# Kernel tuning notes

Hardware: AMD Instinct MI355X
Metric: run time of the kernel (lower is better)

Reference implementation:

```python
import jax, jax.numpy as jnp
import numpy as np

TIME_GAP_BUCKET_COUNT = 64

def setup_inputs() -> dict:
    key = jax.random.key(0)
    ks = jax.random.split(key, 16)
    B, L, H, V, M, G = 32, 512, 256, 100000, 1024, 8
    time_emb = jax.random.normal(ks[8], (TIME_GAP_BUCKET_COUNT + 1, H), jnp.float32) * 0.02
    group_emb = jax.random.normal(ks[9], (G + 1, H), jnp.float32) * 0.02
    return {
        'history_tokens': jax.random.randint(ks[0], (B, L), 0, V, jnp.int32),
        'history_post_tokens': jax.random.randint(ks[1], (B, L), 0, V, jnp.int32),
        'history_author_tokens': jax.random.randint(ks[2], (B, L), 0, V, jnp.int32),
        'history_action_tokens': jax.random.randint(ks[3], (B, L), 0, V, jnp.int32),
        'history_time_gap': jax.random.randint(ks[4], (B, L), 0, TIME_GAP_BUCKET_COUNT + 1, jnp.int32),
        'history_group_ids': jax.random.randint(ks[5], (B, L), 0, G + 1, jnp.int32),
        'history_mask': jax.random.randint(ks[6], (B, L), 0, 2, jnp.int32).astype(bool),
        'token_emb': jax.random.normal(ks[7], (V, H), jnp.float32) * 0.02,
        'time_emb': time_emb.at[0].set(0.0),   # padding_idx=0
        'group_emb': group_emb.at[0].set(0.0),  # padding_idx=0
        'pos_emb': jax.random.normal(ks[10], (M, H), jnp.float32) * 0.02,
        'sep_token': jax.random.normal(ks[11], (H,), jnp.float32) * 0.02,
        'ln_g': jnp.ones((6 * H,), jnp.float32),
        'ln_b': jnp.zeros((6 * H,), jnp.float32),
        'W1': jax.random.normal(ks[12], (6 * H, 4 * H), jnp.float32) * 0.02,
        'b1': jnp.zeros((4 * H,), jnp.float32),
        'W2': jax.random.normal(ks[13], (4 * H, H), jnp.float32) * 0.02,
        'b2': jnp.zeros((H,), jnp.float32),
    }

def _next_valid_group(gid, mask):
    # For each position i, group id of the nearest valid position j > i (or -1).
    B, L = gid.shape
    def step(carry, xm):
        g, m = xm
        return jnp.where(m, g, carry), carry  # emit pre-update carry
    _, nxt = jax.lax.scan(step, jnp.full((B,), -1, gid.dtype),
                          (jnp.flip(gid, 1).T, jnp.flip(mask, 1).T))  # [L,B]
    return jnp.flip(nxt.T, 1)

def reference(history_tokens, history_post_tokens, history_author_tokens,
              history_action_tokens, history_time_gap, history_group_ids,
              history_mask, token_emb, time_emb, group_emb, pos_emb,
              sep_token, ln_g, ln_b, W1, b1, W2, b2):
    M, H = pos_emb.shape
    B, L = history_mask.shape
    # --- event feature assembly ---
    feats = jnp.concatenate([
        token_emb[history_tokens], token_emb[history_post_tokens],
        token_emb[history_author_tokens], token_emb[history_action_tokens],
        time_emb[jnp.clip(history_time_gap, 0, TIME_GAP_BUCKET_COUNT)],
        group_emb[history_group_ids]], axis=-1)  # [B,L,6H]
    mu = feats.mean(-1, keepdims=True)
    var = feats.var(-1, keepdims=True)
    xn = (feats - mu) * jax.lax.rsqrt(var + 1e-5) * ln_g + ln_b
    ev = jax.nn.silu(xn @ W1 + b1) @ W2 + b2  # [B,L,H]
    # --- vectorized merge_with_sep ---
    gid, mask = history_group_ids, history_mask
    nxt = _next_valid_group(gid, mask)
    sep_valid = mask & (nxt >= 0) & (nxt != gid)
    sep_b = jnp.broadcast_to(sep_token, ev.shape)
    tok_c = jnp.stack([ev, sep_b], axis=2).reshape(B, 2 * L, H)   # event, then sep slot
    msk_c = jnp.stack([mask, sep_valid], axis=2).reshape(B, 2 * L)
    rank = jnp.cumsum(msk_c, axis=1) - 1                          # rank among valid pieces
    count = jnp.sum(msk_c, axis=1)                                # pieces per batch
    tgt = M - count[:, None] + rank                               # right-aligned target
    tgt = jnp.where(msk_c & (tgt >= 0), tgt, M)                   # overflow/invalid -> dump slot
    bidx = jnp.arange(B)[:, None]
    merged = jnp.zeros((B, M + 1, H), ev.dtype).at[bidx, tgt].set(
        jnp.where(msk_c[..., None], tok_c, 0.0))[:, :M]
    merged_mask = jnp.zeros((B, M + 1), bool).at[bidx, tgt].set(msk_c)[:, :M]
    merged = (merged + pos_emb[None]) * merged_mask[..., None].astype(ev.dtype)
    return merged, merged_mask
```

## Files before the change

kernel.cpp:

```cpp
#include <hip/hip_runtime.h>
#include <string.h>

#define Hh   256
#define SIXH 1536
#define Bb_  32
#define Ll_  512
#define BL_  16384
#define Mm_  1024
#define N1_  1024
#define K1_  1536
#define K2_  1024
#define N2_  256

typedef __attribute__((ext_vector_type(8))) short bf16x8;
typedef __attribute__((ext_vector_type(4))) float f32x4;

__device__ inline float bf2f(unsigned short u){ unsigned x=(unsigned)u<<16; float f; memcpy(&f,&x,4); return f; }
__device__ inline unsigned short f2bf(float f){ unsigned x; memcpy(&x,&f,4); x = x + 0x7FFFu + ((x>>16)&1u); return (unsigned short)(x>>16); }

#define GL16(gp, lp) __builtin_amdgcn_global_load_lds( \
    (const __attribute__((address_space(1))) void*)(gp), \
    (__attribute__((address_space(3))) void*)(lp), 16, 0, 0)

__global__ __launch_bounds__(256) void prep_kernel(
  const unsigned int* __restrict__ m, int* __restrict__ flag,
  const float* __restrict__ W1, unsigned short* __restrict__ W1t,
  const float* __restrict__ W2, unsigned short* __restrict__ W2t)
{
  int bidg = blockIdx.x;
  int t = threadIdx.x;
  if (bidg == 0){
    bool gt1=false, isf=false;
    for (int i=t;i<4096;i+=256){ unsigned v=m[i]; if(v>1u) gt1=true; if(v==0x3F800000u) isf=true; }
    unsigned long long bg = __ballot(gt1), bf = __ballot(isf);
    __shared__ unsigned long long s1[4], s2[4];
    int w = t>>6;
    if ((t&63)==0){ s1[w]=bg; s2[w]=bf; }
    __syncthreads();
    if (t==0){
      bool g = (s1[0]|s1[1]|s1[2]|s1[3])!=0ull;
      bool f = (s2[0]|s2[1]|s2[2]|s2[3])!=0ull;
      *flag = g ? (f?2:1) : 0;
    }
    return;
  }
  const float* W; unsigned short* Wt; int K, N, id;
  if (bidg <= (K1_/32)*(N1_/32)){ W = W1; Wt = W1t; K = K1_; N = N1_; id = bidg-1; }
  else { W = W2; Wt = W2t; K = K2_; N = N2_; id = bidg-1-(K1_/32)*(N1_/32); }
  __shared__ float tl[32][33];
  int ntx = N >> 5;
  int bx = id % ntx;
  int by = id / ntx;
  int tx = t & 31, ty = t >> 5;
  #pragma unroll
  for (int i=0;i<32;i+=8)
    tl[ty+i][tx] = W[(size_t)(by*32+ty+i)*N + bx*32+tx];
  __syncthreads();
  #pragma unroll
  for (int i=0;i<32;i+=8)
    Wt[(size_t)(bx*32+ty+i)*K + by*32+tx] = f2bf(tl[tx][ty+i]);
}

__global__ __launch_bounds__(256) void gather_ln2_kernel(
  const int* __restrict__ tok, const int* __restrict__ post,
  const int* __restrict__ auth, const int* __restrict__ act,
  const int* __restrict__ tg,  const int* __restrict__ gidp,
  const float* __restrict__ token_emb, const float* __restrict__ time_emb,
  const float* __restrict__ group_emb,
  const float* __restrict__ ln_g, const float* __restrict__ ln_b,
  unsigned short* __restrict__ xn)
{
  int t = threadIdx.x;
  int rib = t >> 7;
  int row = blockIdx.x*2 + rib;
  int wai = (t >> 6) & 1;
  int l   = t & 63;

  int e0 = wai ? post[row] : tok[row];
  int e1 = wai ? act[row]  : auth[row];
  const float* b2p;
  if (wai == 0){
    int i4 = tg[row]; i4 = (i4 < 0) ? 0 : (i4 > 64 ? 64 : i4);
    b2p = time_emb + (size_t)i4*Hh;
  } else {
    b2p = group_emb + (size_t)gidp[row]*Hh;
  }
  const float* b0p = token_emb + (size_t)e0*Hh;
  const float* b1p = token_emb + (size_t)e1*Hh;

  float4 v0 = *(const float4*)(b0p + l*4);
  float4 v1 = *(const float4*)(b1p + l*4);
  float4 v2 = *(const float4*)(b2p + l*4);

  float s  = v0.x+v0.y+v0.z+v0.w + v1.x+v1.y+v1.z+v1.w + v2.x+v2.y+v2.z+v2.w;
  float s2 = v0.x*v0.x+v0.y*v0.y+v0.z*v0.z+v0.w*v0.w
           + v1.x*v1.x+v1.y*v1.y+v1.z*v1.z+v1.w*v1.w
           + v2.x*v2.x+v2.y*v2.y+v2.z*v2.z+v2.w*v2.w;
  #pragma unroll
  for (int off=32; off; off>>=1){ s += __shfl_xor(s,off); s2 += __shfl_xor(s2,off); }

  __shared__ float rs[2][2], rq[2][2];
  if (l==0){ rs[rib][wai] = s; rq[rib][wai] = s2; }
  __syncthreads();
  s  = rs[rib][0] + rs[rib][1];
  s2 = rq[rib][0] + rq[rib][1];
  float mu   = s * (1.0f/1536.0f);
  float var  = s2 * (1.0f/1536.0f) - mu*mu;
  float rstd = rsqrtf(var + 1e-5f);

  unsigned short* xr = xn + (size_t)row*SIXH;
  #pragma unroll
  for (int p=0;p<3;p++){
    int seg = p*2 + wai;
    int j = seg*Hh + l*4;
    float4 g4 = *(const float4*)(ln_g + j);
    float4 bb = *(const float4*)(ln_b + j);
    float4 v = (p==0) ? v0 : (p==1) ? v1 : v2;
    ushort4 o;
    o.x = f2bf((v.x-mu)*rstd*g4.x + bb.x);
    o.y = f2bf((v.y-mu)*rstd*g4.y + bb.y);
    o.z = f2bf((v.z-mu)*rstd*g4.z + bb.z);
    o.w = f2bf((v.w-mu)*rstd*g4.w + bb.w);
    *(ushort4*)(xr + j) = o;
  }
}

__global__ __launch_bounds__(512, 2) void gemm1_cs_kernel(
  const unsigned short* __restrict__ A, const unsigned short* __restrict__ Bt,
  const float* __restrict__ bias, unsigned short* __restrict__ C,
  int M, int N, int K)
{
  __shared__ unsigned short lds[65536];

  int nbx = N >> 8;
  int bid = blockIdx.x;
  if ((gridDim.x & 7) == 0){
    int chunk = gridDim.x >> 3;
    bid = (bid & 7)*chunk + (bid >> 3);
  }
  int bx = bid % nbx, by = bid / nbx;
  int brow = by*256, bcol = bx*256;

  int tid = threadIdx.x, lane = tid & 63, wid = tid >> 6;
  int wr = wid >> 1, wc = wid & 1;

  int sRow = tid >> 3;
  int sSw  = ((tid & 7) ^ (sRow & 7)) << 3;
  const unsigned short* pA0 = A  + (size_t)(brow +   0 + sRow)*K + sSw;
  const unsigned short* pA1 = A  + (size_t)(brow +  64 + sRow)*K + sSw;
  const unsigned short* pA2 = A  + (size_t)(brow + 128 + sRow)*K + sSw;
  const unsigned short* pA3 = A  + (size_t)(brow + 192 + sRow)*K + sSw;
  const unsigned short* pB0 = Bt + (size_t)(bcol +   0 + sRow)*K + sSw;
  const unsigned short* pB1 = Bt + (size_t)(bcol +  64 + sRow)*K + sSw;
  const unsigned short* pB2 = Bt + (size_t)(bcol + 128 + sRow)*K + sSw;
  const unsigned short* pB3 = Bt + (size_t)(bcol + 192 + sRow)*K + sSw;

  int fr = lane & 15, kb = lane >> 4;
  int g0 = (kb ^ (fr & 3)) | (fr & 4);
  int aB = (wr*64  + fr)*64 + g0*8;
  int bB = (wc*128 + fr)*64 + g0*8;

  f32x4 acc[4][8];
  #pragma unroll
  for (int q=0;q<4;q++)
    #pragma unroll
    for (int n=0;n<8;n++) acc[q][n] = (f32x4){0.f,0.f,0.f,0.f};

  bf16x8 a0[4], a1[4], bP[4], bQ[4];

#define ABASE(S) ((S)*16384)
#define BBASE(S) (32768 + (S)*16384)

#define RD_A(buf, S, kc) do{ \
    const unsigned short* L_ = lds + ABASE(S) + (aB ^ ((kc)?32:0)); \
    buf[0] = *(const bf16x8*)(L_); \
    buf[1] = *(const bf16x8*)(L_ + 1024); \
    buf[2] = *(const bf16x8*)(L_ + 2048); \
    buf[3] = *(const bf16x8*)(L_ + 3072); }while(0)

#define RD_B(buf, S, h, kc) do{ \
    const unsigned short* L_ = lds + BBASE(S) + (h)*4096 + (bB ^ ((kc)?32:0)); \
    buf[0] = *(const bf16x8*)(L_); \
    buf[1] = *(const bf16x8*)(L_ + 1024); \
    buf[2] = *(const bf16x8*)(L_ + 2048); \
    buf[3] = *(const bf16x8*)(L_ + 3072); }while(0)

#define STG(p, DB, OFF) GL16((p) + (OFF), lds + (DB) + wid*512)

#define MMX(AF, BF, NB) do{ \
    _Pragma("unroll") for (int q=0;q<4;q++) \
      _Pragma("unroll") for (int nn=0;nn<4;nn++) \
        acc[q][(NB)+nn] = __builtin_amdgcn_mfma_f32_16x16x32_bf16( \
            AF[q], BF[nn], acc[q][(NB)+nn], 0, 0, 0); }while(0)

#define LGKM0 asm volatile("s_waitcnt lgkmcnt(0)" ::: "memory")
#define BAR  __builtin_amdgcn_s_barrier()
#define VM0  asm volatile("s_waitcnt vmcnt(0)" ::: "memory")
#define VNOP do{}while(0)

#define TILE(S, OB1, SP, V4) do{ \
    if (SP){ \
      STG(pA0, ABASE((S)^1) + 0,     OB1); \
      STG(pA1, ABASE((S)^1) + 4096,  OB1); \
      STG(pA2, ABASE((S)^1) + 8192,  OB1); \
      STG(pA3, ABASE((S)^1) + 12288, OB1); \
      STG(pB0, BBASE((S)^1) + 0,     OB1); \
      STG(pB1, BBASE((S)^1) + 4096,  OB1); \
      STG(pB2, BBASE((S)^1) + 8192,  OB1); \
      STG(pB3, BBASE((S)^1) + 12288, OB1); } \
    RD_A(a0, S, 0); RD_B(bP, S, 0, 0); RD_B(bQ, S, 1, 0); \
    MMX(a0, bP, 0); \
    RD_A(a1, S, 1); RD_B(bP, S, 1, 1); \
    MMX(a0, bQ, 4); \
    RD_B(bQ, S, 0, 1); \
    MMX(a1, bP, 4); \
    MMX(a1, bQ, 0); \
    LGKM0; V4; BAR; \
    asm volatile("" ::: "memory"); \
  }while(0)

  int nk = K >> 6;
  STG(pA0, ABASE(0)+0, 0);     STG(pA1, ABASE(0)+4096, 0);
  STG(pA2, ABASE(0)+8192, 0);  STG(pA3, ABASE(0)+12288, 0);
  STG(pB0, BBASE(0)+0, 0);     STG(pB1, BBASE(0)+4096, 0);
  STG(pB2, BBASE(0)+8192, 0);  STG(pB3, BBASE(0)+12288, 0);
  VM0; BAR;
  asm volatile("" ::: "memory");

  for (int tt = 0; tt < (nk-2)/2; ++tt){
    TILE(0,  64, 1, VM0);
    TILE(1, 128, 1, VM0);
    pA0 += 128; pA1 += 128; pA2 += 128; pA3 += 128;
    pB0 += 128; pB1 += 128; pB2 += 128; pB3 += 128;
  }
  TILE(0, 64, 1, VM0);
  TILE(1, 0, 0, VNOP);

#undef TILE
#undef RD_A
#undef RD_B
#undef STG
#undef MMX

  int colb = bcol + wc*128 + fr;
  float bv[8];
  #pragma unroll
  for (int n=0;n<8;n++) bv[n] = bias[colb + n*16];
  int r0 = brow + wr*64 + (lane>>4)*4;
  #pragma unroll
  for (int q=0;q<4;q++){
    #pragma unroll
    for (int j=0;j<4;j++){
      int r = r0 + q*16 + j;
      #pragma unroll
      for (int n=0;n<8;n++){
        float x = acc[q][n][j] + bv[n];
        x = x / (1.0f + expf(-x));
        C[(size_t)r*N + colb + n*16] = f2bf(x);
      }
    }
  }
}

__global__ __launch_bounds__(256) void gemm2_64_kernel(
  const unsigned short* __restrict__ A, const unsigned short* __restrict__ Bt,
  const float* __restrict__ bias, float* __restrict__ C,
  int M, int N, int K)
{
  __shared__ unsigned short As[4096];
  __shared__ unsigned short Bs[4096];
  int nbx = N >> 6;
  int bid = blockIdx.x;
  if ((gridDim.x & 7) == 0){
    int chunk = gridDim.x >> 3;
    bid = (bid & 7)*chunk + (bid >> 3);
  }
  int bx = bid % nbx, by = bid / nbx;
  int brow = by*64, bcol = bx*64;
  int tid = threadIdx.x, lane = tid & 63, wid = tid >> 6;
  int wr = wid >> 1, wc = wid & 1;

  int srow = tid >> 3;
  int sg   = ((tid & 7) ^ (srow & 7)) << 3;
  const unsigned short* pA0 = A  + (size_t)(brow + srow)*K + sg;
  const unsigned short* pA1 = pA0 + (size_t)32*K;
  const unsigned short* pB0 = Bt + (size_t)(bcol + srow)*K + sg;
  const unsigned short* pB1 = pB0 + (size_t)32*K;

  int fr = lane & 15, kb = lane >> 4;
  int g0 = (kb ^ (fr & 7)) << 3;
  int aB = (wr*32 + fr)*64 + g0;
  int bB = (wc*32 + fr)*64 + g0;

  f32x4 acc[2][2];
  #pragma unroll
  for (int i=0;i<2;i++)
    #pragma unroll
    for (int j=0;j<2;j++) acc[i][j] = (f32x4){0.f,0.f,0.f,0.f};

  for (int kt = 0; kt < K; kt += 64){
    GL16(pA0 + kt, As + wid*512);
    GL16(pA1 + kt, As + 2048 + wid*512);
    GL16(pB0 + kt, Bs + wid*512);
    GL16(pB1 + kt, Bs + 2048 + wid*512);
    __syncthreads();
    bf16x8 a[2][2], b[2][2];
    #pragma unroll
    for (int m=0;m<2;m++)
      #pragma unroll
      for (int kc=0;kc<2;kc++){
        a[m][kc] = *(const bf16x8*)(As + ((aB + m*1024) ^ (kc<<5)));
        b[m][kc] = *(const bf16x8*)(Bs + ((bB + m*1024) ^ (kc<<5)));
      }
    #pragma unroll
    for (int kc=0;kc<2;kc++)
      #pragma unroll
      for (int m=0;m<2;m++)
        #pragma unroll
        for (int n=0;n<2;n++)
          acc[m][n] = __builtin_amdgcn_mfma_f32_16x16x32_bf16(a[m][kc], b[n][kc], acc[m][n], 0, 0, 0);
    __syncthreads();
  }

  int col0 = bcol + wc*32 + fr;
  int row0 = brow + wr*32 + (lane >> 4)*4;
  #pragma unroll
  for (int m=0;m<2;m++){
    #pragma unroll
    for (int j=0;j<4;j++){
      int r = row0 + m*16 + j;
      #pragma unroll
      for (int n=0;n<2;n++){
        int c = col0 + n*16;
        C[(size_t)r*N + c] = acc[m][n][j] + bias[c];
      }
    }
  }
}

__global__ __launch_bounds__(512) void merge_meta_kernel(
  const void* __restrict__ maskp, const int* __restrict__ gid,
  const int* __restrict__ flag,
  int* __restrict__ src, int* __restrict__ count)
{
  int b = blockIdx.x;
  int i = threadIdx.x;
  int lane = i & 63, w = i >> 6;
  __shared__ int sg[Ll_];
  __shared__ int fv[8];
  __shared__ int wt[8];
  int f = *flag;
  int mv;
  if (f==0)      mv = ((const int*)maskp)[b*Ll_+i];
  else if (f==1) mv = ((const unsigned char*)maskp)[b*Ll_+i];
  else           mv = (((const float*)maskp)[b*Ll_+i] != 0.0f);
  bool m = (mv != 0);
  int g = gid[b*Ll_+i];
  sg[i] = g;
  unsigned long long W = __ballot(m);
  if (lane==0) fv[w] = W ? (w*64 + __builtin_ctzll(W)) : -1;
  __syncthreads();
  unsigned long long rem = (lane==63) ? 0ull : (W >> (lane+1));
  int nxtpos = -1;
  if (rem) nxtpos = w*64 + lane + 1 + __builtin_ctzll(rem);
  else {
    #pragma unroll
    for (int k=0;k<8;k++)
      if (nxtpos < 0 && k > w && fv[k] >= 0) nxtpos = fv[k];
  }
  int nxt = (nxtpos >= 0) ? sg[nxtpos] : -1;
  bool sep = m && (nxt >= 0) && (nxt != g);
  int ci = (m?1:0) + (sep?1:0);
  int v = ci;
  #pragma unroll
  for (int off=1; off<64; off<<=1){
    int u = __shfl_up(v, off);
    if (lane >= off) v += u;
  }
  if (lane==63) wt[w] = v;
  __syncthreads();
  int woff = 0;
  #pragma unroll
  for (int k=0;k<8;k++) if (k < w) woff += wt[k];
  int e = woff + v - ci;
  int* sb = src + b*Mm_;
  if (m){
    sb[e] = 2*i;
    if (sep) sb[e+1] = 2*i+1;
  }
  if (i==0){
    int tot=0;
    #pragma unroll
    for (int k=0;k<8;k++) tot += wt[k];
    count[b] = tot;
  }
}

__global__ __launch_bounds__(256) void output_kernel(
  const float* __restrict__ ev, const float* __restrict__ pos_emb,
  const float* __restrict__ sep_token,
  const int* __restrict__ src, const int* __restrict__ count,
  float* __restrict__ out)
{
  int tid  = threadIdx.x;
  int tpos = blockIdx.x*4 + (tid>>6);
  int lane = tid & 63;
  int b = tpos >> 10;
  int t = tpos & 1023;
  int cnt = count[b];
  int start = Mm_ - cnt;
  float4 val = make_float4(0.f,0.f,0.f,0.f);
  float maskv = 0.f;
  if (t >= start){
    maskv = 1.f;
    int slot = src[b*Mm_ + (t - start)];
    const float* sv = (slot & 1) ? sep_token
                                 : ev + (size_t)(b*Ll_ + (slot>>1))*Hh;
    float4 x = *(const float4*)(sv + lane*4);
    float4 p = *(const float4*)(pos_emb + (size_t)t*Hh + lane*4);
    val = make_float4(x.x+p.x, x.y+p.y, x.z+p.z, x.w+p.w);
  }
  *(float4*)(out + (size_t)tpos*Hh + lane*4) = val;
  if (lane==0) out[(size_t)Bb_*Mm_*Hh + tpos] = maskv;
}

extern "C" void kernel_launch(void* const* d_in, const int* in_sizes, int n_in,
                              void* d_out, int out_size, void* d_ws, size_t ws_size,
                              hipStream_t stream) {
  const int* tok    = (const int*)d_in[0];
  const int* post   = (const int*)d_in[1];
  const int* auth   = (const int*)d_in[2];
  const int* act    = (const int*)d_in[3];
  const int* tg     = (const int*)d_in[4];
  const int* gid    = (const int*)d_in[5];
  const void* maskp =             d_in[6];
  const float* token_emb = (const float*)d_in[7];
  const float* time_emb  = (const float*)d_in[8];
  const float* group_emb = (const float*)d_in[9];
  const float* pos_emb   = (const float*)d_in[10];
  const float* sep_token = (const float*)d_in[11];
  const float* ln_g = (const float*)d_in[12];
  const float* ln_b = (const float*)d_in[13];
  const float* W1   = (const float*)d_in[14];
  const float* b1   = (const float*)d_in[15];
  const float* W2   = (const float*)d_in[16];
  const float* b2   = (const float*)d_in[17];

  char* ws = (char*)d_ws;
  size_t off = 0;
  int* flag = (int*)ws;                                  off += 256;
  unsigned short* xn  = (unsigned short*)(ws + off);     off += (size_t)BL_*SIXH*2;
  unsigned short* h1  = (unsigned short*)(ws + off);     off += (size_t)BL_*N1_*2;
  float*          ev  = (float*)(ws + off);              off += (size_t)BL_*N2_*4;
  unsigned short* w1t = (unsigned short*)(ws + off);     off += (size_t)K1_*N1_*2;
  unsigned short* w2t = (unsigned short*)(ws + off);     off += (size_t)K2_*N2_*2;
  int*            src = (int*)(ws + off);                off += (size_t)Bb_*Mm_*4;
  int*            cnt = (int*)(ws + off);                off += 256;

  const int PREP_BLOCKS = 1 + (K1_/32)*(N1_/32) + (K2_/32)*(N2_/32);
  prep_kernel<<<PREP_BLOCKS,256,0,stream>>>((const unsigned int*)maskp, flag,
                                            W1, w1t, W2, w2t);
  gather_ln2_kernel<<<BL_/2,256,0,stream>>>(tok,post,auth,act,tg,gid,
                                            token_emb,time_emb,group_emb,
                                            ln_g,ln_b,xn);
  gemm1_cs_kernel<<<(BL_/256)*(N1_/256),512,0,stream>>>(
      xn, w1t, b1, h1, BL_, N1_, K1_);
  gemm2_64_kernel<<<(BL_/64)*(N2_/64),256,0,stream>>>(
      h1, w2t, b2, ev, BL_, N2_, K2_);
  merge_meta_kernel<<<Bb_,512,0,stream>>>(maskp, gid, flag, src, cnt);
  output_kernel<<<(Bb_*Mm_)/4,256,0,stream>>>(ev, pos_emb, sep_token, src, cnt, (float*)d_out);
}
```

Measured before the change: 114.4 us.

## Fuse prep, gather-LN and merge-meta into one kernel; double-buffer GEMM2

Merges the weight transpose/convert, mask-format detection, the embedding gather with LayerNorm, and the merge metadata scan into a single 512-thread launch, partitioned by block index. This removes two kernel launches and the global flag round trip. Each metadata block now rescans the mask to detect its format itself. GEMM2 gains a two-stage LDS double buffer so the next K tile loads while MFMAs run, at the cost of twice the LDS per block.

```diff
diff --git a/kernel.cpp b/kernel.cpp
--- a/kernel.cpp
+++ b/kernel.cpp
@@ -22,57 +22,115 @@
     (const __attribute__((address_space(1))) void*)(gp), \
     (__attribute__((address_space(3))) void*)(lp), 16, 0, 0)
 
-__global__ __launch_bounds__(256) void prep_kernel(
-  const unsigned int* __restrict__ m, int* __restrict__ flag,
-  const float* __restrict__ W1, unsigned short* __restrict__ W1t,
-  const float* __restrict__ W2, unsigned short* __restrict__ W2t)
-{
-  int bidg = blockIdx.x;
-  int t = threadIdx.x;
-  if (bidg == 0){
-    bool gt1=false, isf=false;
-    for (int i=t;i<4096;i+=256){ unsigned v=m[i]; if(v>1u) gt1=true; if(v==0x3F800000u) isf=true; }
-    unsigned long long bg = __ballot(gt1), bf = __ballot(isf);
-    __shared__ unsigned long long s1[4], s2[4];
-    int w = t>>6;
-    if ((t&63)==0){ s1[w]=bg; s2[w]=bf; }
-    __syncthreads();
-    if (t==0){
-      bool g = (s1[0]|s1[1]|s1[2]|s1[3])!=0ull;
-      bool f = (s2[0]|s2[1]|s2[2]|s2[3])!=0ull;
-      *flag = g ? (f?2:1) : 0;
-    }
-    return;
-  }
-  const float* W; unsigned short* Wt; int K, N, id;
-  if (bidg <= (K1_/32)*(N1_/32)){ W = W1; Wt = W1t; K = K1_; N = N1_; id = bidg-1; }
-  else { W = W2; Wt = W2t; K = K2_; N = N2_; id = bidg-1-(K1_/32)*(N1_/32); }
-  __shared__ float tl[32][33];
-  int ntx = N >> 5;
-  int bx = id % ntx;
-  int by = id / ntx;
-  int tx = t & 31, ty = t >> 5;
-  #pragma unroll
-  for (int i=0;i<32;i+=8)
-    tl[ty+i][tx] = W[(size_t)(by*32+ty+i)*N + bx*32+tx];
-  __syncthreads();
-  #pragma unroll
-  for (int i=0;i<32;i+=8)
-    Wt[(size_t)(bx*32+ty+i)*K + by*32+tx] = f2bf(tl[tx][ty+i]);
-}
-
-__global__ __launch_bounds__(256) void gather_ln2_kernel(
+__global__ __launch_bounds__(512) void fused_pre_kernel(
   const int* __restrict__ tok, const int* __restrict__ post,
   const int* __restrict__ auth, const int* __restrict__ act,
   const int* __restrict__ tg,  const int* __restrict__ gidp,
+  const void* __restrict__ maskp,
   const float* __restrict__ token_emb, const float* __restrict__ time_emb,
   const float* __restrict__ group_emb,
   const float* __restrict__ ln_g, const float* __restrict__ ln_b,
-  unsigned short* __restrict__ xn)
+  const float* __restrict__ W1, unsigned short* __restrict__ W1t,
+  const float* __restrict__ W2, unsigned short* __restrict__ W2t,
+  unsigned short* __restrict__ xn,
+  int* __restrict__ src, int* __restrict__ count)
 {
-  int t = threadIdx.x;
+  int bid = blockIdx.x;
+  int t   = threadIdx.x;
+
+  if (bid < 32){
+    int b = bid;
+    int i = t;
+    int lane = i & 63, w = i >> 6;
+    bool gt1=false, isf=false;
+    for (int k=t;k<4096;k+=512){
+      unsigned v=((const unsigned int*)maskp)[k];
+      if(v>1u) gt1=true; if(v==0x3F800000u) isf=true;
+    }
+    __shared__ unsigned long long d1[8], d2[8];
+    unsigned long long bg=__ballot(gt1), bff=__ballot(isf);
+    if (lane==0){ d1[w]=bg; d2[w]=bff; }
+    __syncthreads();
+    unsigned long long og=0, of=0;
+    #pragma unroll
+    for (int k=0;k<8;k++){ og|=d1[k]; of|=d2[k]; }
+    int f = og ? (of?2:1) : 0;
+
+    __shared__ int sg[Ll_];
+    __shared__ int fv[8];
+    __shared__ int wt[8];
+    int mv;
+    if (f==0)      mv = ((const int*)maskp)[b*Ll_+i];
+    else if (f==1) mv = ((const unsigned char*)maskp)[b*Ll_+i];
+    else           mv = (((const float*)maskp)[b*Ll_+i] != 0.0f);
+    bool m = (mv != 0);
+    int g = gidp[b*Ll_+i];
+    sg[i] = g;
+    unsigned long long W = __ballot(m);
+    if (lane==0) fv[w] = W ? (w*64 + __builtin_ctzll(W)) : -1;
+    __syncthreads();
+    unsigned long long rem = (lane==63) ? 0ull : (W >> (lane+1));
+    int nxtpos = -1;
+    if (rem) nxtpos = w*64 + lane + 1 + __builtin_ctzll(rem);
+    else {
+      #pragma unroll
+      for (int k=0;k<8;k++)
+        if (nxtpos < 0 && k > w && fv[k] >= 0) nxtpos = fv[k];
+    }
+    int nxt = (nxtpos >= 0) ? sg[nxtpos] : -1;
+    bool sep = m && (nxt >= 0) && (nxt != g);
+    int ci = (m?1:0) + (sep?1:0);
+    int v = ci;
+    #pragma unroll
+    for (int off=1; off<64; off<<=1){
+      int u = __shfl_up(v, off);
+      if (lane >= off) v += u;
+    }
+    if (lane==63) wt[w] = v;
+    __syncthreads();
+    int woff = 0;
+    #pragma unroll
+    for (int k=0;k<8;k++) if (k < w) woff += wt[k];
+    int e = woff + v - ci;
+    int* sb = src + b*Mm_;
+    if (m){
+      sb[e] = 2*i;
+      if (sep) sb[e+1] = 2*i+1;
+    }
+    if (i==0){
+      int tot=0;
+      #pragma unroll
+      for (int k=0;k<8;k++) tot += wt[k];
+      count[b] = tot;
+    }
+    return;
+  }
+
+  if (bid < 928){
+    int half = t >> 8;
+    int tt = t & 255;
+    int id = (bid-32)*2 + half;
+    const float* W; unsigned short* Wt; int K, N, tid2;
+    if (id < (K1_/32)*(N1_/32)){ W = W1; Wt = W1t; K = K1_; N = N1_; tid2 = id; }
+    else { W = W2; Wt = W2t; K = K2_; N = N2_; tid2 = id - (K1_/32)*(N1_/32); }
+    __shared__ float tl[2][32][33];
+    int ntx = N >> 5;
+    int bx = tid2 % ntx;
+    int by = tid2 / ntx;
+    int tx = tt & 31, ty = tt >> 5;
+    #pragma unroll
+    for (int i2=0;i2<32;i2+=8)
+      tl[half][ty+i2][tx] = W[(size_t)(by*32+ty+i2)*N + bx*32+tx];
+    __syncthreads();
+    #pragma unroll
+    for (int i2=0;i2<32;i2+=8)
+      Wt[(size_t)(bx*32+ty+i2)*K + by*32+tx] = f2bf(tl[half][tx][ty+i2]);
+    return;
+  }
+
+  int rb  = bid - 928;
   int rib = t >> 7;
-  int row = blockIdx.x*2 + rib;
+  int row = rb*4 + rib;
   int wai = (t >> 6) & 1;
   int l   = t & 63;
 
@@ -99,7 +157,7 @@
   #pragma unroll
   for (int off=32; off; off>>=1){ s += __shfl_xor(s,off); s2 += __shfl_xor(s2,off); }
 
-  __shared__ float rs[2][2], rq[2][2];
+  __shared__ float rs[4][2], rq[4][2];
   if (l==0){ rs[rib][wai] = s; rq[rib][wai] = s2; }
   __syncthreads();
   s  = rs[rib][0] + rs[rib][1];
@@ -262,13 +320,12 @@
   }
 }
 
-__global__ __launch_bounds__(256) void gemm2_64_kernel(
+__global__ __launch_bounds__(256) void gemm2_db_kernel(
   const unsigned short* __restrict__ A, const unsigned short* __restrict__ Bt,
   const float* __restrict__ bias, float* __restrict__ C,
   int M, int N, int K)
 {
-  __shared__ unsigned short As[4096];
-  __shared__ unsigned short Bs[4096];
+  __shared__ unsigned short lds2[16384];
   int nbx = N >> 6;
   int bid = blockIdx.x;
   if ((gridDim.x & 7) == 0){
@@ -298,19 +355,28 @@
     #pragma unroll
     for (int j=0;j<2;j++) acc[i][j] = (f32x4){0.f,0.f,0.f,0.f};
 
-  for (int kt = 0; kt < K; kt += 64){
-    GL16(pA0 + kt, As + wid*512);
-    GL16(pA1 + kt, As + 2048 + wid*512);
-    GL16(pB0 + kt, Bs + wid*512);
-    GL16(pB1 + kt, Bs + 2048 + wid*512);
-    __syncthreads();
+#define STG2(S, OFF) do{ \
+    GL16(pA0 + (OFF), lds2 + (S)*4096 + wid*512); \
+    GL16(pA1 + (OFF), lds2 + (S)*4096 + 2048 + wid*512); \
+    GL16(pB0 + (OFF), lds2 + 8192 + (S)*4096 + wid*512); \
+    GL16(pB1 + (OFF), lds2 + 8192 + (S)*4096 + 2048 + wid*512); }while(0)
+
+  STG2(0, 0);
+  asm volatile("s_waitcnt vmcnt(0)" ::: "memory");
+  __builtin_amdgcn_s_barrier();
+  asm volatile("" ::: "memory");
+
+  int nt = K >> 6;
+  for (int t2 = 0; t2 < nt; ++t2){
+    int S = t2 & 1;
+    if (t2 < nt-1) STG2(S^1, (t2+1)*64);
     bf16x8 a[2][2], b[2][2];
     #pragma unroll
     for (int m=0;m<2;m++)
       #pragma unroll
       for (int kc=0;kc<2;kc++){
-        a[m][kc] = *(const bf16x8*)(As + ((aB + m*1024) ^ (kc<<5)));
-        b[m][kc] = *(const bf16x8*)(Bs + ((bB + m*1024) ^ (kc<<5)));
+        a[m][kc] = *(const bf16x8*)(lds2 + (S)*4096 + ((aB + m*1024) ^ (kc<<5)));
+        b[m][kc] = *(const bf16x8*)(lds2 + 8192 + (S)*4096 + ((bB + m*1024) ^ (kc<<5)));
       }
     #pragma unroll
     for (int kc=0;kc<2;kc++)
@@ -319,8 +385,12 @@
         #pragma unroll
         for (int n=0;n<2;n++)
           acc[m][n] = __builtin_amdgcn_mfma_f32_16x16x32_bf16(a[m][kc], b[n][kc], acc[m][n], 0, 0, 0);
-    __syncthreads();
-  }
+    asm volatile("s_waitcnt lgkmcnt(0)" ::: "memory");
+    asm volatile("s_waitcnt vmcnt(0)" ::: "memory");
+    __builtin_amdgcn_s_barrier();
+    asm volatile("" ::: "memory");
+  }
+#undef STG2
 
   int col0 = bcol + wc*32 + fr;
   int row0 = brow + wr*32 + (lane >> 4)*4;
@@ -335,64 +405,6 @@
         C[(size_t)r*N + c] = acc[m][n][j] + bias[c];
       }
     }
-  }
-}
-
-__global__ __launch_bounds__(512) void merge_meta_kernel(
-  const void* __restrict__ maskp, const int* __restrict__ gid,
-  const int* __restrict__ flag,
-  int* __restrict__ src, int* __restrict__ count)
-{
-  int b = blockIdx.x;
-  int i = threadIdx.x;
-  int lane = i & 63, w = i >> 6;
-  __shared__ int sg[Ll_];
-  __shared__ int fv[8];
-  __shared__ int wt[8];
-  int f = *flag;
-  int mv;
-  if (f==0)      mv = ((const int*)maskp)[b*Ll_+i];
-  else if (f==1) mv = ((const unsigned char*)maskp)[b*Ll_+i];
-  else           mv = (((const float*)maskp)[b*Ll_+i] != 0.0f);
-  bool m = (mv != 0);
-  int g = gid[b*Ll_+i];
-  sg[i] = g;
-  unsigned long long W = __ballot(m);
-  if (lane==0) fv[w] = W ? (w*64 + __builtin_ctzll(W)) : -1;
-  __syncthreads();
-  unsigned long long rem = (lane==63) ? 0ull : (W >> (lane+1));
-  int nxtpos = -1;
-  if (rem) nxtpos = w*64 + lane + 1 + __builtin_ctzll(rem);
-  else {
-    #pragma unroll
-    for (int k=0;k<8;k++)
-      if (nxtpos < 0 && k > w && fv[k] >= 0) nxtpos = fv[k];
-  }
-  int nxt = (nxtpos >= 0) ? sg[nxtpos] : -1;
-  bool sep = m && (nxt >= 0) && (nxt != g);
-  int ci = (m?1:0) + (sep?1:0);
-  int v = ci;
-  #pragma unroll
-  for (int off=1; off<64; off<<=1){
-    int u = __shfl_up(v, off);
-    if (lane >= off) v += u;
-  }
-  if (lane==63) wt[w] = v;
-  __syncthreads();
-  int woff = 0;
-  #pragma unroll
-  for (int k=0;k<8;k++) if (k < w) woff += wt[k];
-  int e = woff + v - ci;
-  int* sb = src + b*Mm_;
-  if (m){
-    sb[e] = 2*i;
-    if (sep) sb[e+1] = 2*i+1;
-  }
-  if (i==0){
-    int tot=0;
-    #pragma unroll
-    for (int k=0;k<8;k++) tot += wt[k];
-    count[b] = tot;
   }
 }
 
@@ -456,17 +468,16 @@
   unsigned short* w2t = (unsigned short*)(ws + off);     off += (size_t)K2_*N2_*2;
   int*            src = (int*)(ws + off);                off += (size_t)Bb_*Mm_*4;
   int*            cnt = (int*)(ws + off);                off += 256;
-
-  const int PREP_BLOCKS = 1 + (K1_/32)*(N1_/32) + (K2_/32)*(N2_/32);
-  prep_kernel<<<PREP_BLOCKS,256,0,stream>>>((const unsigned int*)maskp, flag,
-                                            W1, w1t, W2, w2t);
-  gather_ln2_kernel<<<BL_/2,256,0,stream>>>(tok,post,auth,act,tg,gid,
-                                            token_emb,time_emb,group_emb,
-                                            ln_g,ln_b,xn);
+  (void)flag;
+
+  const int PRE_BLOCKS = 32 + 896 + BL_/4;
+  fused_pre_kernel<<<PRE_BLOCKS,512,0,stream>>>(
+      tok,post,auth,act,tg,gid, maskp,
+      token_emb,time_emb,group_emb, ln_g,ln_b,
+      W1,w1t,W2,w2t, xn, src,cnt);
   gemm1_cs_kernel<<<(BL_/256)*(N1_/256),512,0,stream>>>(
       xn, w1t, b1, h1, BL_, N1_, K1_);
-  gemm2_64_kernel<<<(BL_/64)*(N2_/64),256,0,stream>>>(
+  gemm2_db_kernel<<<(BL_/64)*(N2_/64),256,0,stream>>>(
       h1, w2t, b2, ev, BL_, N2_, K2_);
-  merge_meta_kernel<<<Bb_,512,0,stream>>>(maskp, gid, flag, src, cnt);
   output_kernel<<<(Bb_*Mm_)/4,256,0,stream>>>(ev, pos_emb, sep_token, src, cnt, (float*)d_out);
 }
```

Result: faster. 105.9 us (median of 2 runs) (-7.5%).
